# Kernel optimization log

Hardware: AMD Instinct MI355X
Metric: run time of the kernel (lower is better)

## Reference

```python
import jax, jax.numpy as jnp
import numpy as np
from jax import lax

DIM, N_STATE, DT_RANK = 1024, 16, 64
BATCH, SEQ = 2, 2048


def setup_inputs() -> dict:
    key = jax.random.key(0)
    ks = jax.random.split(key, 12)
    s = 0.02
    x = jax.random.normal(ks[0], (BATCH, SEQ, DIM), dtype=jnp.float32)
    in_proj_w = jax.random.normal(ks[1], (2 * DIM, DIM), dtype=jnp.float32) * s
    conv_w = jax.random.normal(ks[2], (DIM, 1, 3), dtype=jnp.float32) * s
    conv_b = jax.random.normal(ks[3], (DIM,), dtype=jnp.float32) * s
    A_log = jax.random.normal(ks[4], (DIM, N_STATE), dtype=jnp.float32) * s
    D_param = jax.random.normal(ks[5], (DIM,), dtype=jnp.float32) * s
    x_proj_w = jax.random.normal(ks[6], (DT_RANK + 2 * N_STATE, DIM), dtype=jnp.float32) * s
    # dt_proj init mimics the torch module: bias = inv-softplus of dt in [dt_min, dt_max]
    dt = jnp.exp(jax.random.uniform(ks[7], (DIM,)) * (np.log(0.1) - np.log(0.001)) + np.log(0.001))
    dt = jnp.clip(dt, 0.0001, None)
    inv_dt = dt + jnp.log(-jnp.expm1(-dt))
    dt_init_std = DT_RANK ** (-0.5)
    dt_proj_w = jnp.tile(inv_dt[:, None], (1, DT_RANK)) * dt_init_std
    dt_proj_b = inv_dt
    out_proj_w = jax.random.normal(ks[8], (DIM, DIM), dtype=jnp.float32) * s
    return {
        "x": x, "in_proj_w": in_proj_w, "conv_w": conv_w, "conv_b": conv_b,
        "A_log": A_log, "D_param": D_param, "x_proj_w": x_proj_w,
        "dt_proj_w": dt_proj_w, "dt_proj_b": dt_proj_b, "out_proj_w": out_proj_w,
    }


def _selective_scan(u, delta, A, Bp, Cp, D_param):
    # u, delta: (B, L, D); A: (D, N); Bp, Cp: (B, L, N)
    deltaA = jnp.exp(delta[..., None] * A)                       # (B, L, D, N)
    deltaB_u = delta[..., None] * Bp[:, :, None, :] * u[..., None]  # (B, L, D, N)

    def step(state, inputs):
        dA_t, dBu_t, C_t = inputs          # (B, D, N), (B, D, N), (B, N)
        state = dA_t * state + dBu_t       # (B, D, N)
        y_t = jnp.einsum("bdn,bn->bd", state, C_t)
        return state, y_t

    init = jnp.zeros((u.shape[0], u.shape[2], A.shape[1]), dtype=u.dtype)
    xs = (jnp.swapaxes(deltaA, 0, 1), jnp.swapaxes(deltaB_u, 0, 1), jnp.swapaxes(Cp, 0, 1))
    _, ys = lax.scan(step, init, xs)       # ys: (L, B, D)
    y = jnp.swapaxes(ys, 0, 1)             # (B, L, D)
    return y + u * D_param


def reference(x, in_proj_w, conv_w, conv_b, A_log, D_param, x_proj_w, dt_proj_w, dt_proj_b, out_proj_w):
    B, L, D = x.shape
    xz = x @ in_proj_w.T                   # (B, L, 2D)
    xc, z = jnp.split(xz, 2, axis=-1)
    # depthwise conv1d, kernel 3, padding 1 (output length == L)
    xc = jnp.swapaxes(xc, 1, 2)            # (B, D, L)
    xc = lax.conv_general_dilated(
        xc, conv_w, window_strides=(1,), padding=[(1, 1)],
        dimension_numbers=("NCH", "OIH", "NCH"), feature_group_count=D,
    ) + conv_b[None, :, None]
    xc = jnp.swapaxes(xc, 1, 2)            # (B, L, D)
    x_dbl = xc @ x_proj_w.T                # (B, L, dt_rank + 2N)
    dt_r, Bp, Cp = jnp.split(x_dbl, [DT_RANK, DT_RANK + N_STATE], axis=-1)
    delta = jax.nn.softplus(dt_r @ dt_proj_w.T + dt_proj_b)   # (B, L, D)
    A = -jnp.exp(A_log)                    # (D, N)
    y = _selective_scan(xc, delta, A, Bp, Cp, D_param)
    y = y * jax.nn.silu(z)
    return y @ out_proj_w.T
```

## Files before the change

kernel.cpp:

```cpp
#include <hip/hip_runtime.h>
#include <math.h>

#define BATCH 2
#define SEQ   2048
#define DIM   1024
#define NST   16
#define DTR   64
#define KSL   8

typedef _Float16 f16x8 __attribute__((ext_vector_type(8)));
typedef float f32x4 __attribute__((ext_vector_type(4)));

__device__ __forceinline__ float softplus_f(float v) {
  return fmaxf(v, 0.f) + log1pf(expf(-fabsf(v)));
}

__device__ __forceinline__ void gl_lds16(const _Float16* g, _Float16* l) {
  __builtin_amdgcn_global_load_lds(
      (const __attribute__((address_space(1))) void*)g,
      (__attribute__((address_space(3))) void*)l, 16, 0, 0);
}

template <int CTRL, int RMASK>
__device__ __forceinline__ float dpp_mov(float oldv, float src) {
  return __int_as_float(__builtin_amdgcn_update_dpp(
      __float_as_int(oldv), __float_as_int(src), CTRL, RMASK, 0xf, false));
}

#define FMA_ROW(i, av)                                        \
  acc[i][0] = fmaf(av, b.x, acc[i][0]);                       \
  acc[i][1] = fmaf(av, b.y, acc[i][1]);                       \
  acc[i][2] = fmaf(av, b.z, acc[i][2]);                       \
  acc[i][3] = fmaf(av, b.w, acc[i][3]);

__global__ __launch_bounds__(256) void k_cvt3(
    const float* __restrict__ in0, _Float16* __restrict__ hi0,
    _Float16* __restrict__ lo0,
    const float* __restrict__ in1, _Float16* __restrict__ hi1,
    _Float16* __restrict__ lo1,
    const float* __restrict__ in2, _Float16* __restrict__ hi2,
    _Float16* __restrict__ lo2) {
  int bb = blockIdx.x;
  const float* in;
  _Float16 *hi, *lo;
  if (bb < 2048) {
    in = in0; hi = hi0; lo = lo0;
  } else if (bb < 3072) {
    in = in1; hi = hi1; lo = lo1; bb -= 2048;
  } else {
    in = in2; hi = hi2; lo = lo2; bb -= 3072;
  }
  const int i = (bb * 256 + threadIdx.x) * 8;
  const float4 a = *(const float4*)(in + i);
  const float4 b = *(const float4*)(in + i + 4);
  const float v[8] = {a.x, a.y, a.z, a.w, b.x, b.y, b.z, b.w};
  f16x8 h, l;
#pragma unroll
  for (int j = 0; j < 8; ++j) {
    const _Float16 hh = (_Float16)v[j];
    h[j] = hh;
    l[j] = (_Float16)(v[j] - (float)hh);
  }
  *(f16x8*)(hi + i) = h;
  *(f16x8*)(lo + i) = l;
}

template <int EPI>
__global__ __launch_bounds__(256) void kgemm_f16x3(
    const _Float16* __restrict__ Ah, const _Float16* __restrict__ Al,
    const _Float16* __restrict__ Bh, const _Float16* __restrict__ Bl,
    float* __restrict__ out0, float* __restrict__ out1) {
  __shared__ _Float16 sm[32768];
  const int tid = threadIdx.x;
  const int wid = tid >> 6, lane = tid & 63;
  const int wm = wid >> 1, wn = wid & 1;
  const int m0 = blockIdx.y * 128;
  const int n0 = blockIdx.x * 128;

  const int r0 = wid * 32;
  const int srow = lane >> 2;
  const int skqs = ((lane & 3) ^ ((lane >> 3) & 3)) * 8;
  const _Float16* gAh = Ah + (size_t)(m0 + r0 + srow) * 1024 + skqs;
  const _Float16* gAl = Al + (size_t)(m0 + r0 + srow) * 1024 + skqs;
  const _Float16* gBh = Bh + (size_t)(n0 + r0 + srow) * 1024 + skqs;
  const _Float16* gBl = Bl + (size_t)(n0 + r0 + srow) * 1024 + skqs;

  const int fr = lane & 15;
  const int fks = (((lane >> 4) ^ ((fr >> 1) & 3))) * 8;

  f32x4 acc[4][4];
#pragma unroll
  for (int i = 0; i < 4; ++i)
#pragma unroll
    for (int j = 0; j < 4; ++j) acc[i][j] = (f32x4)(0.f);

  auto STAGE = [&](int buf, int k0) {
    _Float16* base = sm + buf * 16384;
    _Float16* lA = base + r0 * 32;
    gl_lds16(gAh + k0, lA);
    gl_lds16(gAh + k0 + 16 * 1024, lA + 512);
    gl_lds16(gAl + k0, lA + 4096);
    gl_lds16(gAl + k0 + 16 * 1024, lA + 4096 + 512);
    gl_lds16(gBh + k0, lA + 8192);
    gl_lds16(gBh + k0 + 16 * 1024, lA + 8192 + 512);
    gl_lds16(gBl + k0, lA + 12288);
    gl_lds16(gBl + k0 + 16 * 1024, lA + 12288 + 512);
  };

  STAGE(0, 0);
  int cur = 0;
  for (int k0 = 0; k0 < 1024; k0 += 32) {
    __syncthreads();
    if (k0 + 32 < 1024) STAGE(cur ^ 1, k0 + 32);
    const _Float16* base = sm + cur * 16384;

    f16x8 ah[4], alo[4], bh[4], blo[4];
#pragma unroll
    for (int i = 0; i < 4; ++i) {
      const int ao = (wm * 64 + i * 16 + fr) * 32 + fks;
      const int bo = (wn * 64 + i * 16 + fr) * 32 + fks;
      ah[i]  = *(const f16x8*)(base + ao);
      alo[i] = *(const f16x8*)(base + 4096 + ao);
      bh[i]  = *(const f16x8*)(base + 8192 + bo);
      blo[i] = *(const f16x8*)(base + 12288 + bo);
    }
#pragma unroll
    for (int i = 0; i < 4; ++i)
#pragma unroll
      for (int j = 0; j < 4; ++j) {
        acc[i][j] = __builtin_amdgcn_mfma_f32_16x16x32_f16(ah[i], bh[j],
                                                           acc[i][j], 0, 0, 0);
        acc[i][j] = __builtin_amdgcn_mfma_f32_16x16x32_f16(ah[i], blo[j],
                                                           acc[i][j], 0, 0, 0);
        acc[i][j] = __builtin_amdgcn_mfma_f32_16x16x32_f16(alo[i], bh[j],
                                                           acc[i][j], 0, 0, 0);
      }
    cur ^= 1;
  }

  const int lr4 = (lane >> 4) * 4, lc = lane & 15;
#pragma unroll
  for (int i = 0; i < 4; ++i) {
#pragma unroll
    for (int j = 0; j < 4; ++j) {
      const int ar = m0 + wm * 64 + i * 16 + lr4;
      const int bc = n0 + wn * 64 + j * 16 + lc;
#pragma unroll
      for (int r = 0; r < 4; ++r) {
        const float v = acc[i][j][r];
        if (EPI == 0) {
          out0[(size_t)(ar + r) * 1024 + bc] = v;
        } else {
          const int bb = bc >> 11, tt = bc & 2047;
          if (ar < 1024) {
            out0[((size_t)bb * 1024 + ar + r) * 2048 + tt] = v;
          } else {
            out1[((size_t)bb * 1024 + (ar + r - 1024)) * 2048 + tt] = v;
          }
        }
      }
    }
  }
}

__global__ __launch_bounds__(256) void k_conv(
    const float* __restrict__ xcraw, const float* __restrict__ cw,
    const float* __restrict__ cb, float* __restrict__ xc) {
  const int idx = blockIdx.x * 256 + threadIdx.x;
  const int t0 = (idx & (SEQ / 4 - 1)) * 4;
  const int r = idx >> 9;
  const int d = r & (DIM - 1);
  const float w0 = cw[d * 3 + 0], w1 = cw[d * 3 + 1], w2 = cw[d * 3 + 2];
  const float bias = cb[d];
  const float* in = xcraw + (size_t)r * SEQ;
  float o[4];
#pragma unroll
  for (int j = 0; j < 4; ++j) {
    const int t = t0 + j;
    const float xm = (t > 0) ? in[t - 1] : 0.f;
    const float x0 = in[t];
    const float xp = (t < SEQ - 1) ? in[t + 1] : 0.f;
    o[j] = fmaf(w0, xm, fmaf(w1, x0, fmaf(w2, xp, bias)));
  }
  *(float4*)(xc + (size_t)r * SEQ + t0) = make_float4(o[0], o[1], o[2], o[3]);
}

__global__ __launch_bounds__(256) void k2_xproj_sk(
    const float* __restrict__ xc, const float* __restrict__ wp,
    float* __restrict__ part) {
  __shared__ float As[16][100];
  __shared__ float Bs[16][68];
  const int tid = threadIdx.x;
  const int tile = blockIdx.x;
  const int ks = blockIdx.y;
  const int b = tile >> 5;
  const int t0 = (tile & 31) * 64;
  const int kbase = ks * (DIM / KSL);
  const int tx = tid & 15, ty = tid >> 4;
  float acc[6][4] = {{0.f}};
  for (int k = 0; k < DIM / KSL; k += 16) {
    float a_reg[6];
#pragma unroll
    for (int i = 0; i < 6; ++i) {
      const int ii = tid + 256 * i;
      a_reg[i] = wp[(size_t)(ii >> 4) * DIM + kbase + k + (ii & 15)];
    }
    const int krow = tid >> 4, t4 = (tid & 15) * 4;
    const float4 b_reg = *(const float4*)(
        xc + ((size_t)b * DIM + kbase + k + krow) * SEQ + t0 + t4);
    __syncthreads();
#pragma unroll
    for (int i = 0; i < 6; ++i) {
      const int ii = tid + 256 * i;
      As[ii & 15][ii >> 4] = a_reg[i];
    }
    *(float4*)&Bs[krow][t4] = b_reg;
    __syncthreads();
#pragma unroll
    for (int kk = 0; kk < 16; ++kk) {
      const float4 bA = *(const float4*)&Bs[kk][tx * 4];
#pragma unroll
      for (int i = 0; i < 6; ++i) {
        const float a = As[kk][ty + 16 * i];
        acc[i][0] = fmaf(a, bA.x, acc[i][0]);
        acc[i][1] = fmaf(a, bA.y, acc[i][1]);
        acc[i][2] = fmaf(a, bA.z, acc[i][2]);
        acc[i][3] = fmaf(a, bA.w, acc[i][3]);
      }
    }
    __syncthreads();
  }
#pragma unroll
  for (int i = 0; i < 6; ++i) {
    const int j = ty + 16 * i;
    const size_t o = ((size_t)(ks * BATCH + b) * 96 + j) * SEQ + t0;
    *(float4*)(part + o + tx * 4) =
        make_float4(acc[i][0], acc[i][1], acc[i][2], acc[i][3]);
  }
}

__global__ __launch_bounds__(256) void k_red(const float* __restrict__ part,
                                             float* __restrict__ xdbl) {
  const size_t PL = (size_t)BATCH * 96 * SEQ;
  const size_t i4 = ((size_t)blockIdx.x * 256 + threadIdx.x) * 4;
  float4 s = *(const float4*)(part + i4);
#pragma unroll
  for (int ks = 1; ks < KSL; ++ks) {
    const float4 v = *(const float4*)(part + ks * PL + i4);
    s.x += v.x; s.y += v.y; s.z += v.z; s.w += v.w;
  }
  *(float4*)(xdbl + i4) = s;
}

__global__ __launch_bounds__(256) void k3_dtproj(
    const float* __restrict__ xdbl, const float* __restrict__ dtw,
    const float* __restrict__ dtb, float* __restrict__ delta) {
  __shared__ float As[16][68];
  __shared__ float Bs[16][68];
  const int tid = threadIdx.x;
  const int b = blockIdx.z;
  const int d0 = blockIdx.y * 64;
  const int t0 = blockIdx.x * 64;
  const int tx = tid & 15, ty = tid >> 4;
  const int lrow = tid >> 2, lcol = (tid & 3) * 4;
  const int bk = tid >> 4, bt4 = (tid & 15) * 4;
  float acc[4][4] = {{0.f}};
  for (int k = 0; k < DTR; k += 16) {
    const float4 av =
        *(const float4*)(dtw + (size_t)(d0 + lrow) * DTR + k + lcol);
    const float4 bv =
        *(const float4*)(xdbl + ((size_t)b * 96 + k + bk) * SEQ + t0 + bt4);
    __syncthreads();
    As[lcol + 0][lrow] = av.x; As[lcol + 1][lrow] = av.y;
    As[lcol + 2][lrow] = av.z; As[lcol + 3][lrow] = av.w;
    Bs[bk][bt4 + 0] = bv.x; Bs[bk][bt4 + 1] = bv.y;
    Bs[bk][bt4 + 2] = bv.z; Bs[bk][bt4 + 3] = bv.w;
    __syncthreads();
#pragma unroll
    for (int kk = 0; kk < 16; ++kk) {
      const float4 a = *(const float4*)&As[kk][ty * 4];
      const float4 b = *(const float4*)&Bs[kk][tx * 4];
      FMA_ROW(0, a.x) FMA_ROW(1, a.y) FMA_ROW(2, a.z) FMA_ROW(3, a.w)
    }
  }
#pragma unroll
  for (int i = 0; i < 4; ++i) {
    const int d = d0 + ty * 4 + i;
    const float bias = dtb[d];
    float4 v;
    v.x = softplus_f(acc[i][0] + bias);
    v.y = softplus_f(acc[i][1] + bias);
    v.z = softplus_f(acc[i][2] + bias);
    v.w = softplus_f(acc[i][3] + bias);
    *(float4*)(delta + ((size_t)b * DIM + d) * SEQ + t0 + tx * 4) = v;
  }
}

__global__ __launch_bounds__(1024) void k_scan_fused(
    const float* __restrict__ delta, const float* __restrict__ u,
    const float* __restrict__ xdbl, const float* __restrict__ A_log,
    const float* __restrict__ Dp, const float* __restrict__ z,
    float* __restrict__ y) {
  __shared__ float red[2][NST][2][260];
  const int tid = threadIdx.x;
  const int wv = tid >> 6;
  const int lane = tid & 63;
  const int idx = blockIdx.x;
  const int b = idx >> 10, d = idx & (DIM - 1);
  const float A = -expf(A_log[d * NST + wv]);
  const float Dprm = Dp[d];
  const float* drow = delta + (size_t)idx * SEQ;
  const float* urow = u + (size_t)idx * SEQ;
  const float* Brow = xdbl + ((size_t)b * 96 + DTR + wv) * SEQ;
  const float* Crow = xdbl + ((size_t)b * 96 + DTR + NST + wv) * SEQ;
  const float* zrow = z + (size_t)idx * SEQ;
  float* yrow = y + (size_t)idx * SEQ;
  float s_c = 0.f;
  const int tl = lane * 8;
  const int tl2 = lane * 4;

  float4 dA = *(const float4*)(drow + tl);
  float4 dB = *(const float4*)(drow + tl + 4);
  float4 uA = *(const float4*)(urow + tl);
  float4 uB = *(const float4*)(urow + tl + 4);
  float4 bA = *(const float4*)(Brow + tl);
  float4 bB = *(const float4*)(Brow + tl + 4);
  float uRc = 0.f, zRc = 0.f;
  if (tid < 512) { uRc = urow[tid]; zRc = zrow[tid]; }

  for (int w = 0; w < SEQ / 512; ++w) {
    const int t0 = w * 512;
    const float4 cA = *(const float4*)(Crow + t0 + tl);
    const float4 cB = *(const float4*)(Crow + t0 + tl + 4);
    float uRn = 0.f, zRn = 0.f;
    if (w + 1 < SEQ / 512 && tid < 512) {
      uRn = urow[t0 + 512 + tid];
      zRn = zrow[t0 + 512 + tid];
    }
    float p[8], q[8];
    {
      const float dls[8] = {dA.x, dA.y, dA.z, dA.w, dB.x, dB.y, dB.z, dB.w};
      const float us[8]  = {uA.x, uA.y, uA.z, uA.w, uB.x, uB.y, uB.z, uB.w};
      const float Bb[8]  = {bA.x, bA.y, bA.z, bA.w, bB.x, bB.y, bB.z, bB.w};
      p[0] = __expf(dls[0] * A);
      q[0] = dls[0] * us[0] * Bb[0];
#pragma unroll
      for (int i = 1; i < 8; ++i) {
        const float a = __expf(dls[i] * A);
        const float bq = dls[i] * us[i] * Bb[i];
        p[i] = a * p[i - 1];
        q[i] = fmaf(a, q[i - 1], bq);
      }
    }
    if (w + 1 < SEQ / 512) {
      const int tn = t0 + 512 + tl;
      dA = *(const float4*)(drow + tn);
      dB = *(const float4*)(drow + tn + 4);
      uA = *(const float4*)(urow + tn);
      uB = *(const float4*)(urow + tn + 4);
      bA = *(const float4*)(Brow + tn);
      bB = *(const float4*)(Brow + tn + 4);
    }
    float ia = p[7], ib = q[7];
    {
      float oa, ob;
      oa = dpp_mov<0x111, 0xf>(1.f, ia);
      ob = dpp_mov<0x111, 0xf>(0.f, ib);
      ib = fmaf(ia, ob, ib); ia *= oa;
      oa = dpp_mov<0x112, 0xf>(1.f, ia);
      ob = dpp_mov<0x112, 0xf>(0.f, ib);
      ib = fmaf(ia, ob, ib); ia *= oa;
      oa = dpp_mov<0x114, 0xf>(1.f, ia);
      ob = dpp_mov<0x114, 0xf>(0.f, ib);
      ib = fmaf(ia, ob, ib); ia *= oa;
      oa = dpp_mov<0x118, 0xf>(1.f, ia);
      ob = dpp_mov<0x118, 0xf>(0.f, ib);
      ib = fmaf(ia, ob, ib); ia *= oa;
      oa = dpp_mov<0x142, 0xa>(1.f, ia);
      ob = dpp_mov<0x142, 0xa>(0.f, ib);
      ib = fmaf(ia, ob, ib); ia *= oa;
      oa = dpp_mov<0x143, 0xc>(1.f, ia);
      ob = dpp_mov<0x143, 0xc>(0.f, ib);
      ib = fmaf(ia, ob, ib); ia *= oa;
    }
    const float Wa = __shfl(ia, 63, 64);
    const float Wb = __shfl(ib, 63, 64);
    float ea = __shfl_up(ia, 1, 64);
    float eb = __shfl_up(ib, 1, 64);
    if (lane == 0) { ea = 1.f; eb = 0.f; }
    const float S = fmaf(ea, s_c, eb);
    s_c = fmaf(Wa, s_c, Wb);
    float4 y0, y1;
    y0.x = fmaf(p[0], S, q[0]) * cA.x;
    y0.y = fmaf(p[1], S, q[1]) * cA.y;
    y0.z = fmaf(p[2], S, q[2]) * cA.z;
    y0.w = fmaf(p[3], S, q[3]) * cA.w;
    y1.x = fmaf(p[4], S, q[4]) * cB.x;
    y1.y = fmaf(p[5], S, q[5]) * cB.y;
    y1.z = fmaf(p[6], S, q[6]) * cB.z;
    y1.w = fmaf(p[7], S, q[7]) * cB.w;
    *(float4*)&red[w & 1][wv][0][tl2] = y0;
    *(float4*)&red[w & 1][wv][1][tl2] = y1;
    __syncthreads();
    if (tid < 512) {
      const int sub = (tid >> 2) & 1;
      const int pos = ((tid >> 3) << 2) | (tid & 3);
      float sum = 0.f;
#pragma unroll
      for (int nn = 0; nn < NST; ++nn) sum += red[w & 1][nn][sub][pos];
      sum = fmaf(uRc, Dprm, sum);
      const float sg = __builtin_amdgcn_rcpf(1.f + __expf(-zRc));
      yrow[t0 + tid] = sum * zRc * sg;
    }
    uRc = uRn;
    zRc = zRn;
  }
}

__global__ __launch_bounds__(256) void k_gt(
    const float* __restrict__ y, _Float16* __restrict__ gh,
    _Float16* __restrict__ gl) {
  __shared__ _Float16 th[64][68];
  __shared__ _Float16 tl[64][68];
  const int ti = threadIdx.x;
  const int t0 = blockIdx.x * 64;
  const int d0 = blockIdx.y * 64;
  const int b = blockIdx.z;
  const int c4 = (ti & 15) * 4;
#pragma unroll
  for (int rr = 0; rr < 4; ++rr) {
    const int dl_ = (ti >> 4) + 16 * rr;
    const size_t base = ((size_t)b * DIM + d0 + dl_) * SEQ + t0 + c4;
    const float4 yv = *(const float4*)(y + base);
    const float gy[4] = {yv.x, yv.y, yv.z, yv.w};
#pragma unroll
    for (int k = 0; k < 4; ++k) {
      const _Float16 h = (_Float16)gy[k];
      th[dl_][c4 + k] = h;
      tl[dl_][c4 + k] = (_Float16)(gy[k] - (float)h);
    }
  }
  __syncthreads();
#pragma unroll
  for (int rr = 0; rr < 2; ++rr) {
    const int chunk = ti + 256 * rr;
    const int tloc = chunk >> 3;
    const int dchunk = (chunk & 7) * 8;
    f16x8 hv, lv;
#pragma unroll
    for (int j = 0; j < 8; ++j) {
      hv[j] = th[dchunk + j][tloc];
      lv[j] = tl[dchunk + j][tloc];
    }
    const size_t o = ((size_t)b * SEQ + t0 + tloc) * DIM + d0 + dchunk;
    *(f16x8*)(gh + o) = hv;
    *(f16x8*)(gl + o) = lv;
  }
}

extern "C" void kernel_launch(void* const* d_in, const int* in_sizes, int n_in,
                              void* d_out, int out_size, void* d_ws,
                              size_t ws_size, hipStream_t stream) {
  const float* x          = (const float*)d_in[0];
  const float* in_proj_w  = (const float*)d_in[1];
  const float* conv_w     = (const float*)d_in[2];
  const float* conv_b     = (const float*)d_in[3];
  const float* A_log      = (const float*)d_in[4];
  const float* D_param    = (const float*)d_in[5];
  const float* x_proj_w   = (const float*)d_in[6];
  const float* dt_proj_w  = (const float*)d_in[7];
  const float* dt_proj_b  = (const float*)d_in[8];
  const float* out_proj_w = (const float*)d_in[9];
  float* out = (float*)d_out;
  float* ws = (float*)d_ws;

  const size_t PLANE = (size_t)BATCH * SEQ * DIM;
  float* xcraw = ws;
  float* delta = ws;
  _Float16* gh = (_Float16*)ws;
  _Float16* gl = (_Float16*)ws + PLANE;
  float* xc    = ws + PLANE;
  float* zbuf  = ws + 2 * PLANE;
  _Float16* xh = (_Float16*)(ws + 3 * PLANE);
  _Float16* xl = xh + PLANE;
  float* part  = ws + 3 * PLANE;
  float* ybuf  = ws + 3 * PLANE;
  float* xdbl  = ws + 4 * PLANE;
  _Float16* wih = (_Float16*)(ws + 4 * PLANE + 1572864);
  _Float16* wil = wih + (size_t)2 * DIM * DIM;
  _Float16* woh = wil + (size_t)2 * DIM * DIM;
  _Float16* wol = woh + (size_t)DIM * DIM;

  k_cvt3<<<dim3(3584), 256, 0, stream>>>(x, xh, xl, in_proj_w, wih, wil,
                                         out_proj_w, woh, wol);

  kgemm_f16x3<1><<<dim3(32, 16), 256, 0, stream>>>(wih, wil, xh, xl,
                                                   xcraw, zbuf);
  k_conv<<<dim3((BATCH * DIM * SEQ / 4) / 256), 256, 0, stream>>>(
      xcraw, conv_w, conv_b, xc);
  k2_xproj_sk<<<dim3(64, KSL), 256, 0, stream>>>(xc, x_proj_w, part);
  k_red<<<dim3(384), 256, 0, stream>>>(part, xdbl);
  k3_dtproj<<<dim3(SEQ / 64, DIM / 64, BATCH), 256, 0, stream>>>(
      xdbl, dt_proj_w, dt_proj_b, delta);
  k_scan_fused<<<dim3(BATCH * DIM), 1024, 0, stream>>>(
      delta, xc, xdbl, A_log, D_param, zbuf, ybuf);
  k_gt<<<dim3(SEQ / 64, DIM / 64, BATCH), 256, 0, stream>>>(ybuf, gh, gl);
  kgemm_f16x3<0><<<dim3(8, 32), 256, 0, stream>>>(gh, gl, woh, wol,
                                                  out, nullptr);
}
```

Before: 286.2 us.

## Fuse x fp32-to-f16 hi/lo split into in_proj GEMM B-operand staging

Drops the separate conversion of the activation x into f16 hi/lo planes. The in_proj GEMM now loads fp32 x tiles into registers, splits them into hi/lo f16 and writes them into swizzled LDS, with a custom waitcnt+barrier and register prefetch two steps ahead. This saves a full read and write pass over x (plus a re-read of the f16 copies). The cost is extra VALU work and register pressure inside the GEMM, and a more complex sync schedule.

```diff
diff --git a/kernel.cpp b/kernel.cpp
--- a/kernel.cpp
+++ b/kernel.cpp
@@ -21,6 +21,13 @@
       (__attribute__((address_space(3))) void*)l, 16, 0, 0);
 }
 
+__device__ __forceinline__ void raw_lds_barrier() {
+  asm volatile("s_waitcnt lgkmcnt(0)" ::: "memory");
+  __builtin_amdgcn_sched_barrier(0);
+  __builtin_amdgcn_s_barrier();
+  __builtin_amdgcn_sched_barrier(0);
+}
+
 template <int CTRL, int RMASK>
 __device__ __forceinline__ float dpp_mov(float oldv, float src) {
   return __int_as_float(__builtin_amdgcn_update_dpp(
@@ -33,9 +40,7 @@
   acc[i][2] = fmaf(av, b.z, acc[i][2]);                       \
   acc[i][3] = fmaf(av, b.w, acc[i][3]);
 
-__global__ __launch_bounds__(256) void k_cvt3(
-    const float* __restrict__ in0, _Float16* __restrict__ hi0,
-    _Float16* __restrict__ lo0,
+__global__ __launch_bounds__(256) void k_cvt2(
     const float* __restrict__ in1, _Float16* __restrict__ hi1,
     _Float16* __restrict__ lo1,
     const float* __restrict__ in2, _Float16* __restrict__ hi2,
@@ -43,12 +48,10 @@
   int bb = blockIdx.x;
   const float* in;
   _Float16 *hi, *lo;
-  if (bb < 2048) {
-    in = in0; hi = hi0; lo = lo0;
-  } else if (bb < 3072) {
-    in = in1; hi = hi1; lo = lo1; bb -= 2048;
+  if (bb < 1024) {
+    in = in1; hi = hi1; lo = lo1;
   } else {
-    in = in2; hi = hi2; lo = lo2; bb -= 3072;
+    in = in2; hi = hi2; lo = lo2; bb -= 1024;
   }
   const int i = (bb * 256 + threadIdx.x) * 8;
   const float4 a = *(const float4*)(in + i);
@@ -69,6 +72,7 @@
 __global__ __launch_bounds__(256) void kgemm_f16x3(
     const _Float16* __restrict__ Ah, const _Float16* __restrict__ Al,
     const _Float16* __restrict__ Bh, const _Float16* __restrict__ Bl,
+    const float* __restrict__ Bx,
     float* __restrict__ out0, float* __restrict__ out1) {
   __shared__ _Float16 sm[32768];
   const int tid = threadIdx.x;
@@ -82,8 +86,6 @@
   const int skqs = ((lane & 3) ^ ((lane >> 3) & 3)) * 8;
   const _Float16* gAh = Ah + (size_t)(m0 + r0 + srow) * 1024 + skqs;
   const _Float16* gAl = Al + (size_t)(m0 + r0 + srow) * 1024 + skqs;
-  const _Float16* gBh = Bh + (size_t)(n0 + r0 + srow) * 1024 + skqs;
-  const _Float16* gBl = Bl + (size_t)(n0 + r0 + srow) * 1024 + skqs;
 
   const int fr = lane & 15;
   const int fks = (((lane >> 4) ^ ((fr >> 1) & 3))) * 8;
@@ -94,48 +96,134 @@
 #pragma unroll
     for (int j = 0; j < 4; ++j) acc[i][j] = (f32x4)(0.f);
 
-  auto STAGE = [&](int buf, int k0) {
-    _Float16* base = sm + buf * 16384;
-    _Float16* lA = base + r0 * 32;
-    gl_lds16(gAh + k0, lA);
-    gl_lds16(gAh + k0 + 16 * 1024, lA + 512);
-    gl_lds16(gAl + k0, lA + 4096);
-    gl_lds16(gAl + k0 + 16 * 1024, lA + 4096 + 512);
-    gl_lds16(gBh + k0, lA + 8192);
-    gl_lds16(gBh + k0 + 16 * 1024, lA + 8192 + 512);
-    gl_lds16(gBl + k0, lA + 12288);
-    gl_lds16(gBl + k0 + 16 * 1024, lA + 12288 + 512);
-  };
-
-  STAGE(0, 0);
-  int cur = 0;
-  for (int k0 = 0; k0 < 1024; k0 += 32) {
-    __syncthreads();
-    if (k0 + 32 < 1024) STAGE(cur ^ 1, k0 + 32);
-    const _Float16* base = sm + cur * 16384;
-
-    f16x8 ah[4], alo[4], bh[4], blo[4];
-#pragma unroll
-    for (int i = 0; i < 4; ++i) {
-      const int ao = (wm * 64 + i * 16 + fr) * 32 + fks;
-      const int bo = (wn * 64 + i * 16 + fr) * 32 + fks;
-      ah[i]  = *(const f16x8*)(base + ao);
-      alo[i] = *(const f16x8*)(base + 4096 + ao);
-      bh[i]  = *(const f16x8*)(base + 8192 + bo);
-      blo[i] = *(const f16x8*)(base + 12288 + bo);
-    }
-#pragma unroll
-    for (int i = 0; i < 4; ++i)
-#pragma unroll
-      for (int j = 0; j < 4; ++j) {
-        acc[i][j] = __builtin_amdgcn_mfma_f32_16x16x32_f16(ah[i], bh[j],
-                                                           acc[i][j], 0, 0, 0);
-        acc[i][j] = __builtin_amdgcn_mfma_f32_16x16x32_f16(ah[i], blo[j],
-                                                           acc[i][j], 0, 0, 0);
-        acc[i][j] = __builtin_amdgcn_mfma_f32_16x16x32_f16(alo[i], bh[j],
-                                                           acc[i][j], 0, 0, 0);
-      }
-    cur ^= 1;
+  if constexpr (EPI == 0) {
+    const _Float16* gBh = Bh + (size_t)(n0 + r0 + srow) * 1024 + skqs;
+    const _Float16* gBl = Bl + (size_t)(n0 + r0 + srow) * 1024 + skqs;
+    auto STAGE = [&](int buf, int k0) {
+      _Float16* base = sm + buf * 16384;
+      _Float16* lA = base + r0 * 32;
+      gl_lds16(gAh + k0, lA);
+      gl_lds16(gAh + k0 + 16 * 1024, lA + 512);
+      gl_lds16(gAl + k0, lA + 4096);
+      gl_lds16(gAl + k0 + 16 * 1024, lA + 4096 + 512);
+      gl_lds16(gBh + k0, lA + 8192);
+      gl_lds16(gBh + k0 + 16 * 1024, lA + 8192 + 512);
+      gl_lds16(gBl + k0, lA + 12288);
+      gl_lds16(gBl + k0 + 16 * 1024, lA + 12288 + 512);
+    };
+    STAGE(0, 0);
+    int cur = 0;
+    for (int k0 = 0; k0 < 1024; k0 += 32) {
+      __syncthreads();
+      if (k0 + 32 < 1024) STAGE(cur ^ 1, k0 + 32);
+      const _Float16* base = sm + cur * 16384;
+      f16x8 ah[4], alo[4], bh[4], blo[4];
+#pragma unroll
+      for (int i = 0; i < 4; ++i) {
+        const int ao = (wm * 64 + i * 16 + fr) * 32 + fks;
+        const int bo = (wn * 64 + i * 16 + fr) * 32 + fks;
+        ah[i]  = *(const f16x8*)(base + ao);
+        alo[i] = *(const f16x8*)(base + 4096 + ao);
+        bh[i]  = *(const f16x8*)(base + 8192 + bo);
+        blo[i] = *(const f16x8*)(base + 12288 + bo);
+      }
+#pragma unroll
+      for (int i = 0; i < 4; ++i)
+#pragma unroll
+        for (int j = 0; j < 4; ++j) {
+          acc[i][j] = __builtin_amdgcn_mfma_f32_16x16x32_f16(
+              ah[i], bh[j], acc[i][j], 0, 0, 0);
+          acc[i][j] = __builtin_amdgcn_mfma_f32_16x16x32_f16(
+              ah[i], blo[j], acc[i][j], 0, 0, 0);
+          acc[i][j] = __builtin_amdgcn_mfma_f32_16x16x32_f16(
+              alo[i], bh[j], acc[i][j], 0, 0, 0);
+        }
+      cur ^= 1;
+    }
+  } else {
+    const float* gBx =
+        Bx + (size_t)(n0 + r0 + srow) * 1024 + (lane & 3) * 8;
+    const int wchunk = skqs;
+    float4 brg[4];
+
+    auto LOADB = [&](int k0) {
+      brg[0] = *(const float4*)(gBx + k0);
+      brg[1] = *(const float4*)(gBx + k0 + 4);
+      brg[2] = *(const float4*)(gBx + k0 + 16 * 1024);
+      brg[3] = *(const float4*)(gBx + k0 + 16 * 1024 + 4);
+    };
+    auto STAGE_A = [&](int buf, int k0) {
+      _Float16* base = sm + buf * 16384;
+      _Float16* lA = base + r0 * 32;
+      gl_lds16(gAh + k0, lA);
+      gl_lds16(gAh + k0 + 16 * 1024, lA + 512);
+      gl_lds16(gAl + k0, lA + 4096);
+      gl_lds16(gAl + k0 + 16 * 1024, lA + 4096 + 512);
+    };
+    auto WRITEB = [&](int buf) {
+      _Float16* bB = sm + buf * 16384 + 8192 + r0 * 32;
+#pragma unroll
+      for (int h = 0; h < 2; ++h) {
+        const float v[8] = {brg[2 * h].x,     brg[2 * h].y,
+                            brg[2 * h].z,     brg[2 * h].w,
+                            brg[2 * h + 1].x, brg[2 * h + 1].y,
+                            brg[2 * h + 1].z, brg[2 * h + 1].w};
+        f16x8 hv, lv;
+#pragma unroll
+        for (int j = 0; j < 8; ++j) {
+          const _Float16 hh = (_Float16)v[j];
+          hv[j] = hh;
+          lv[j] = (_Float16)(v[j] - (float)hh);
+        }
+        const int off = (srow + 16 * h) * 32 + wchunk;
+        *(f16x8*)(bB + off) = hv;
+        *(f16x8*)(bB + 4096 + off) = lv;
+      }
+    };
+
+    LOADB(0);
+    STAGE_A(0, 0);
+    __syncthreads();
+    WRITEB(0);
+    LOADB(32);
+    STAGE_A(1, 32);
+    raw_lds_barrier();
+
+    int cur = 0;
+    for (int k = 0; k < 32; ++k) {
+      const _Float16* base = sm + cur * 16384;
+      f16x8 ah[4], alo[4], bh[4], blo[4];
+#pragma unroll
+      for (int i = 0; i < 4; ++i) {
+        const int ao = (wm * 64 + i * 16 + fr) * 32 + fks;
+        const int bo = (wn * 64 + i * 16 + fr) * 32 + fks;
+        ah[i]  = *(const f16x8*)(base + ao);
+        alo[i] = *(const f16x8*)(base + 4096 + ao);
+        bh[i]  = *(const f16x8*)(base + 8192 + bo);
+        blo[i] = *(const f16x8*)(base + 12288 + bo);
+      }
+#pragma unroll
+      for (int i = 0; i < 4; ++i)
+#pragma unroll
+        for (int j = 0; j < 4; ++j) {
+          acc[i][j] = __builtin_amdgcn_mfma_f32_16x16x32_f16(
+              ah[i], bh[j], acc[i][j], 0, 0, 0);
+          acc[i][j] = __builtin_amdgcn_mfma_f32_16x16x32_f16(
+              ah[i], blo[j], acc[i][j], 0, 0, 0);
+          acc[i][j] = __builtin_amdgcn_mfma_f32_16x16x32_f16(
+              alo[i], bh[j], acc[i][j], 0, 0, 0);
+        }
+      if (k < 31) {
+        __syncthreads();
+        WRITEB(cur ^ 1);
+        if (k + 2 < 32) {
+          LOADB((k + 2) * 32);
+          STAGE_A(cur, (k + 2) * 32);
+        }
+        raw_lds_barrier();
+      }
+      cur ^= 1;
+    }
   }
 
   const int lr4 = (lane >> 4) * 4, lc = lane & 15;
@@ -481,8 +569,6 @@
   _Float16* gl = (_Float16*)ws + PLANE;
   float* xc    = ws + PLANE;
   float* zbuf  = ws + 2 * PLANE;
-  _Float16* xh = (_Float16*)(ws + 3 * PLANE);
-  _Float16* xl = xh + PLANE;
   float* part  = ws + 3 * PLANE;
   float* ybuf  = ws + 3 * PLANE;
   float* xdbl  = ws + 4 * PLANE;
@@ -491,11 +577,11 @@
   _Float16* woh = wil + (size_t)2 * DIM * DIM;
   _Float16* wol = woh + (size_t)DIM * DIM;
 
-  k_cvt3<<<dim3(3584), 256, 0, stream>>>(x, xh, xl, in_proj_w, wih, wil,
+  k_cvt2<<<dim3(1536), 256, 0, stream>>>(in_proj_w, wih, wil,
                                          out_proj_w, woh, wol);
 
-  kgemm_f16x3<1><<<dim3(32, 16), 256, 0, stream>>>(wih, wil, xh, xl,
-                                                   xcraw, zbuf);
+  kgemm_f16x3<1><<<dim3(32, 16), 256, 0, stream>>>(wih, wil, nullptr, nullptr,
+                                                   x, xcraw, zbuf);
   k_conv<<<dim3((BATCH * DIM * SEQ / 4) / 256), 256, 0, stream>>>(
       xcraw, conv_w, conv_b, xc);
   k2_xproj_sk<<<dim3(64, KSL), 256, 0, stream>>>(xc, x_proj_w, part);
@@ -505,6 +591,6 @@
   k_scan_fused<<<dim3(BATCH * DIM), 1024, 0, stream>>>(
       delta, xc, xdbl, A_log, D_param, zbuf, ybuf);
   k_gt<<<dim3(SEQ / 64, DIM / 64, BATCH), 256, 0, stream>>>(ybuf, gh, gl);
-  kgemm_f16x3<0><<<dim3(8, 32), 256, 0, stream>>>(gh, gl, woh, wol,
+  kgemm_f16x3<0><<<dim3(8, 32), 256, 0, stream>>>(gh, gl, woh, wol, nullptr,
                                                   out, nullptr);
 }
```

Measured after the change: 285.8 us. Within noise of the previous version (-0.1%).
